# Kernel tuning notes

Hardware: AMD Instinct MI355X
Metric: run time of the kernel (lower is better)

The kernel has to match this reference:

```python
import jax, jax.numpy as jnp
import numpy as np

N_NODES = 100000
N_EDGES = 1600000
D_IN = 128
D_OUT = 128
EPS = 1e-5


def setup_inputs() -> dict:
    key = jax.random.key(0)
    ks = jax.random.split(key, 5)
    x = jax.random.normal(ks[0], (N_NODES, D_IN), dtype=jnp.float32)
    edge_index = jax.random.randint(ks[1], (2, N_EDGES), 0, N_NODES, dtype=jnp.int64)
    scale = 1.0 / np.sqrt(D_IN)
    W_root = jax.random.normal(ks[2], (D_IN, D_OUT), dtype=jnp.float32) * scale
    W_rel = jax.random.normal(ks[3], (D_IN, D_OUT), dtype=jnp.float32) * scale
    b_rel = jax.random.normal(ks[4], (D_OUT,), dtype=jnp.float32) * 0.01
    gamma = jnp.ones((D_OUT,), dtype=jnp.float32)
    beta = jnp.zeros((D_OUT,), dtype=jnp.float32)
    return {"x": x, "edge_index": edge_index, "W_root": W_root, "W_rel": W_rel,
            "b_rel": b_rel, "gamma": gamma, "beta": beta}


def reference(x, edge_index, W_root, W_rel, b_rel, gamma, beta):
    # GraphConv: out = aggr(x_j) @ W_rel + b_rel + x @ W_root   (aggr = sum)
    src = edge_index[0]
    dst = edge_index[1]
    aggr = jax.ops.segment_sum(x[src], dst, num_segments=x.shape[0])  # [N, D_IN]
    h = aggr @ W_rel + b_rel + x @ W_root                              # [N, D_OUT]
    # NodeLevelBatchNorm (training mode: batch stats over node dim, biased var)
    mean = jnp.mean(h, axis=0)
    var = jnp.mean(jnp.square(h - mean), axis=0)
    h_norm = (h - mean) * jax.lax.rsqrt(var + EPS) * gamma + beta
    return jax.nn.relu(h_norm)
```

## Files before the change

### kernel.cpp

```cpp
#include <hip/hip_runtime.h>

#define N_NODES 100000
#define N_EDGES 1600000
#define D 128
#define NB 196
#define EPT 10
#define CHUNK 2560
#define BIN_BLOCKS 625
#define CVT_X_BLOCKS 6250
#define ZROW N_NODES
#define PBK 13312

typedef __bf16 bf16x8 __attribute__((ext_vector_type(8)));
typedef float f32x4 __attribute__((ext_vector_type(4)));

__device__ __forceinline__ unsigned f2bf(float f) {
    unsigned u = __float_as_uint(f);
    return (u + 0x7fffu + ((u >> 16) & 1u)) >> 16;
}
__device__ __forceinline__ float bf_lo(unsigned u) { return __uint_as_float(u << 16); }
__device__ __forceinline__ float bf_hi(unsigned u) { return __uint_as_float(u & 0xffff0000u); }

__global__ __launch_bounds__(256) void prep_kernel(const float* __restrict__ x,
                                                   const float* __restrict__ Wrel,
                                                   const float* __restrict__ Wroot,
                                                   const int* __restrict__ ei,
                                                   unsigned short* __restrict__ x_bf,
                                                   unsigned short* __restrict__ Wt,
                                                   int* __restrict__ bcount) {
    __shared__ int h[256];
    int b = blockIdx.x;
    int t = threadIdx.x;
    if (b < CVT_X_BLOCKS) {
        size_t i = ((size_t)b * 256 + t) * 8;
        float4 v0 = *(const float4*)(x + i);
        float4 v1 = *(const float4*)(x + i + 4);
        uint4 p;
        p.x = f2bf(v0.x) | (f2bf(v0.y) << 16);
        p.y = f2bf(v0.z) | (f2bf(v0.w) << 16);
        p.z = f2bf(v1.x) | (f2bf(v1.y) << 16);
        p.w = f2bf(v1.z) | (f2bf(v1.w) << 16);
        *(uint4*)(x_bf + i) = p;
    } else if (b < CVT_X_BLOCKS + 128) {
        int c = b - CVT_X_BLOCKS;
        float v = (t < 128) ? Wrel[t * D + c] : Wroot[(t - 128) * D + c];
        Wt[c * 256 + t] = (unsigned short)f2bf(v);
    } else if (b == CVT_X_BLOCKS + 128) {
        if (t < 16) *(uint4*)(x_bf + (size_t)ZROW * D + t * 8) = make_uint4(0, 0, 0, 0);
    } else {
        int blk = b - (CVT_X_BLOCKS + 129);
        h[t] = 0;
        __syncthreads();
        int base = blk * CHUNK;
#pragma unroll
        for (int i = 0; i < EPT; ++i) {
            int dst = ei[N_EDGES + base + i * 256 + t];
            atomicAdd(&h[dst >> 9], 1);
        }
        __syncthreads();
        if (t < NB && h[t]) atomicAdd(&bcount[t], h[t]);
    }
}

__global__ __launch_bounds__(256) void bscan_kernel(const int* __restrict__ bcount,
                                                    int* __restrict__ bucket_base,
                                                    int* __restrict__ bcur) {
    __shared__ int s[256];
    int t = threadIdx.x;
    int v = (t < NB) ? bcount[t] : 0;
    s[t] = v;
    __syncthreads();
    for (int off = 1; off < 256; off <<= 1) {
        int a = (t >= off) ? s[t - off] : 0;
        __syncthreads();
        s[t] += a;
        __syncthreads();
    }
    int excl = s[t] - v;
    if (t < NB) {
        bucket_base[t] = excl;
        bcur[t] = excl;
    }
    if (t == NB) bucket_base[NB] = N_EDGES;
}

__global__ __launch_bounds__(256) void binify_kernel(const int* __restrict__ ei,
                                                     int* __restrict__ bcur,
                                                     unsigned* __restrict__ epk) {
    __shared__ int lhist[256];
    __shared__ int lstart[256];
    __shared__ int lfill[256];
    __shared__ int gbase[256];
    __shared__ uint2 stage[CHUNK];

    int t = threadIdx.x;
    int base = blockIdx.x * CHUNK;
    lhist[t] = 0;
    lfill[t] = 0;
    __syncthreads();

    int src[EPT], dst[EPT];
#pragma unroll
    for (int i = 0; i < EPT; ++i) {
        int e = base + i * 256 + t;
        src[i] = ei[e];
        dst[i] = ei[N_EDGES + e];
        atomicAdd(&lhist[dst[i] >> 9], 1);
    }
    __syncthreads();

    int v = lhist[t];
    lstart[t] = v;
    __syncthreads();
    for (int off = 1; off < 256; off <<= 1) {
        int a = (t >= off) ? lstart[t - off] : 0;
        __syncthreads();
        lstart[t] += a;
        __syncthreads();
    }
    int excl = lstart[t] - v;
    if (t < NB && v > 0) gbase[t] = atomicAdd(&bcur[t], v);
    __syncthreads();
    lstart[t] = excl;
    __syncthreads();

#pragma unroll
    for (int i = 0; i < EPT; ++i) {
        int b = dst[i] >> 9;
        int lp = atomicAdd(&lfill[b], 1);
        stage[lstart[b] + lp] = make_uint2((unsigned)src[i], (unsigned)dst[i]);
    }
    __syncthreads();

    for (int i = t; i < CHUNK; i += 256) {
        uint2 p = stage[i];
        int b = (int)(p.y >> 9);
        unsigned code = p.x | ((p.y & 511u) << 17);
        epk[gbase[b] + (i - lstart[b])] = code;
    }
}

__global__ __launch_bounds__(256) void place_kernel(const unsigned* __restrict__ epk,
                                                    const int* __restrict__ bucket_base,
                                                    int* __restrict__ rbeg,
                                                    int* __restrict__ rend,
                                                    int* __restrict__ srcs) {
    __shared__ int cnt[512];
    __shared__ int sA[512];
    __shared__ int sB[512];
    __shared__ int cursor[512];
    int b = blockIdx.x;
    int t = threadIdx.x;
    int pbeg = bucket_base[b];
    int pend = bucket_base[b + 1];
    int R = b * PBK;

    cnt[t] = 0;
    cnt[t + 256] = 0;
    __syncthreads();
    for (int i = pbeg + t; i < pend; i += 256)
        atomicAdd(&cnt[epk[i] >> 17], 1);
    __syncthreads();

    for (int j = t; j < 512; j += 256) sA[j] = j ? ((cnt[j - 1] + 7) & ~7) : 0;
    __syncthreads();
    int* cur = sA;
    int* nxt = sB;
    for (int off = 1; off < 512; off <<= 1) {
        for (int j = t; j < 512; j += 256)
            nxt[j] = cur[j] + ((j >= off) ? cur[j - off] : 0);
        __syncthreads();
        int* tm = cur; cur = nxt; nxt = tm;
    }

    for (int j = t; j < 512; j += 256) {
        int pj = (cnt[j] + 7) & ~7;
        int s = R + cur[j];
        int g = (b << 9) + j;
        if (g < 100352) { rbeg[g] = s; rend[g] = s + pj; }
        cursor[j] = s;
    }
    __syncthreads();

    for (int i = pbeg + t; i < pend; i += 256) {
        unsigned code = epk[i];
        int pos = atomicAdd(&cursor[code >> 17], 1);
        srcs[pos] = (int)(code & 0x1FFFFu);
    }
    __syncthreads();

    for (int j = t; j < 512; j += 256) {
        int endp = R + cur[j] + ((cnt[j] + 7) & ~7);
        for (int p = cursor[j]; p < endp; ++p) srcs[p] = ZROW;
    }
}

__global__ __launch_bounds__(256) void fused_gemm(const unsigned short* __restrict__ x_bf,
                                                  const int* __restrict__ rbeg,
                                                  const int* __restrict__ rend,
                                                  const int* __restrict__ srcs,
                                                  const unsigned short* __restrict__ Wt,
                                                  const float* __restrict__ brel,
                                                  unsigned short* __restrict__ h_bf,
                                                  float* __restrict__ gsum,
                                                  float* __restrict__ gss) {
    __shared__ unsigned short Af[2048 * 8];
    __shared__ unsigned short Bf[2048 * 8];
    __shared__ float sbias[128];
    __shared__ float SredS[4][128];
    __shared__ float SredQ[4][128];

    const int t = threadIdx.x;
    const int wave = t >> 6;
    const int lane = t & 63;
    const int quad = lane >> 4;
    const int l16 = lane & 15;
    const int blockRow = blockIdx.x * 128;

    if (t < 128) sbias[t] = brel[t];

#pragma unroll
    for (int f = t; f < 2048; f += 256) {
        int kcl = f >> 9;
        int ct = (f >> 6) & 7;
        int ln = f & 63;
        int col = ct * 16 + (ln & 15);
        int kb = kcl * 32 + ((ln >> 4) << 3);
        *(uint4*)&Bf[f * 8] = *(const uint4*)(Wt + col * 256 + kb);
    }

    const unsigned short* xp = x_bf + l16 * 8;
#pragma unroll 1
    for (int g = 0; g < 8; ++g) {
        int r = wave * 32 + g * 4 + quad;
        int node = blockRow + r;
        int e = rbeg[node];
        int end = rend[node];
        float a0 = 0.f, a1 = 0.f, a2 = 0.f, a3 = 0.f;
        float a4 = 0.f, a5 = 0.f, a6 = 0.f, a7 = 0.f;
        for (; e < end; e += 8) {
            int4 s0 = *(const int4*)(srcs + e);
            int4 s1 = *(const int4*)(srcs + e + 4);
            uint4 u0 = *(const uint4*)(xp + (size_t)s0.x * D);
            uint4 u1 = *(const uint4*)(xp + (size_t)s0.y * D);
            uint4 u2 = *(const uint4*)(xp + (size_t)s0.z * D);
            uint4 u3 = *(const uint4*)(xp + (size_t)s0.w * D);
            uint4 u4 = *(const uint4*)(xp + (size_t)s1.x * D);
            uint4 u5 = *(const uint4*)(xp + (size_t)s1.y * D);
            uint4 u6 = *(const uint4*)(xp + (size_t)s1.z * D);
            uint4 u7 = *(const uint4*)(xp + (size_t)s1.w * D);
            a0 += bf_lo(u0.x) + bf_lo(u1.x) + bf_lo(u2.x) + bf_lo(u3.x)
                + bf_lo(u4.x) + bf_lo(u5.x) + bf_lo(u6.x) + bf_lo(u7.x);
            a1 += bf_hi(u0.x) + bf_hi(u1.x) + bf_hi(u2.x) + bf_hi(u3.x)
                + bf_hi(u4.x) + bf_hi(u5.x) + bf_hi(u6.x) + bf_hi(u7.x);
            a2 += bf_lo(u0.y) + bf_lo(u1.y) + bf_lo(u2.y) + bf_lo(u3.y)
                + bf_lo(u4.y) + bf_lo(u5.y) + bf_lo(u6.y) + bf_lo(u7.y);
            a3 += bf_hi(u0.y) + bf_hi(u1.y) + bf_hi(u2.y) + bf_hi(u3.y)
                + bf_hi(u4.y) + bf_hi(u5.y) + bf_hi(u6.y) + bf_hi(u7.y);
            a4 += bf_lo(u0.z) + bf_lo(u1.z) + bf_lo(u2.z) + bf_lo(u3.z)
                + bf_lo(u4.z) + bf_lo(u5.z) + bf_lo(u6.z) + bf_lo(u7.z);
            a5 += bf_hi(u0.z) + bf_hi(u1.z) + bf_hi(u2.z) + bf_hi(u3.z)
                + bf_hi(u4.z) + bf_hi(u5.z) + bf_hi(u6.z) + bf_hi(u7.z);
            a6 += bf_lo(u0.w) + bf_lo(u1.w) + bf_lo(u2.w) + bf_lo(u3.w)
                + bf_lo(u4.w) + bf_lo(u5.w) + bf_lo(u6.w) + bf_lo(u7.w);
            a7 += bf_hi(u0.w) + bf_hi(u1.w) + bf_hi(u2.w) + bf_hi(u3.w)
                + bf_hi(u4.w) + bf_hi(u5.w) + bf_hi(u6.w) + bf_hi(u7.w);
        }
        uint4 w;
        w.x = f2bf(a0) | (f2bf(a1) << 16);
        w.y = f2bf(a2) | (f2bf(a3) << 16);
        w.z = f2bf(a4) | (f2bf(a5) << 16);
        w.w = f2bf(a6) | (f2bf(a7) << 16);
        int c = l16;
        int wf = ((r >> 5) << 3) + (((r >> 4) & 1) << 2) + (c >> 2);
        int L = ((c & 3) << 4) + (r & 15);
        *(uint4*)&Af[(wf * 64 + L) * 8] = w;
    }
    __syncthreads();

    f32x4 acc[2][8];
#pragma unroll
    for (int i = 0; i < 2; ++i)
#pragma unroll
        for (int j = 0; j < 8; ++j) acc[i][j] = (f32x4){0.f, 0.f, 0.f, 0.f};

#pragma unroll
    for (int kcl = 0; kcl < 4; ++kcl) {
        bf16x8 af0 = *(const bf16x8*)&Af[(((wave << 3) + kcl) * 64 + lane) * 8];
        bf16x8 af1 = *(const bf16x8*)&Af[(((wave << 3) + 4 + kcl) * 64 + lane) * 8];
#pragma unroll
        for (int ct = 0; ct < 8; ++ct) {
            bf16x8 bfrag = *(const bf16x8*)&Bf[((kcl * 8 + ct) * 64 + lane) * 8];
            acc[0][ct] = __builtin_amdgcn_mfma_f32_16x16x32_bf16(af0, bfrag, acc[0][ct], 0, 0, 0);
            acc[1][ct] = __builtin_amdgcn_mfma_f32_16x16x32_bf16(af1, bfrag, acc[1][ct], 0, 0, 0);
        }
    }
    __syncthreads();

#pragma unroll
    for (int f = t; f < 2048; f += 256) {
        int kcl = f >> 9;
        int ct = (f >> 6) & 7;
        int ln = f & 63;
        int col = ct * 16 + (ln & 15);
        int kb = 128 + kcl * 32 + ((ln >> 4) << 3);
        *(uint4*)&Bf[f * 8] = *(const uint4*)(Wt + col * 256 + kb);
    }
    __syncthreads();

    const int rowb = blockRow + wave * 32;
#pragma unroll
    for (int kcl = 0; kcl < 4; ++kcl) {
        const int k0 = kcl * 32 + quad * 8;
        bf16x8 af0 = *(const bf16x8*)(x_bf + (size_t)(rowb + l16) * D + k0);
        bf16x8 af1 = *(const bf16x8*)(x_bf + (size_t)(rowb + 16 + l16) * D + k0);
#pragma unroll
        for (int ct = 0; ct < 8; ++ct) {
            bf16x8 bfrag = *(const bf16x8*)&Bf[((kcl * 8 + ct) * 64 + lane) * 8];
            acc[0][ct] = __builtin_amdgcn_mfma_f32_16x16x32_bf16(af0, bfrag, acc[0][ct], 0, 0, 0);
            acc[1][ct] = __builtin_amdgcn_mfma_f32_16x16x32_bf16(af1, bfrag, acc[1][ct], 0, 0, 0);
        }
    }

    float csum[8], css[8];
#pragma unroll
    for (int ct = 0; ct < 8; ++ct) { csum[ct] = 0.f; css[ct] = 0.f; }

#pragma unroll
    for (int rt = 0; rt < 2; ++rt) {
#pragma unroll
        for (int ct = 0; ct < 8; ++ct) {
            int col = ct * 16 + l16;
            float bv = sbias[col];
#pragma unroll
            for (int reg = 0; reg < 4; ++reg) {
                int row = blockRow + wave * 32 + rt * 16 + quad * 4 + reg;
                if (row < N_NODES) {
                    float v = acc[rt][ct][reg] + bv;
                    h_bf[(size_t)row * D + col] = (unsigned short)f2bf(v);
                    csum[ct] += v;
                    css[ct] += v * v;
                }
            }
        }
    }
#pragma unroll
    for (int ct = 0; ct < 8; ++ct) {
        float s = csum[ct], q = css[ct];
        s += __shfl_xor(s, 16);
        s += __shfl_xor(s, 32);
        q += __shfl_xor(q, 16);
        q += __shfl_xor(q, 32);
        if (quad == 0) {
            SredS[wave][ct * 16 + l16] = s;
            SredQ[wave][ct * 16 + l16] = q;
        }
    }
    __syncthreads();
    if (t < 128) {
        float s = SredS[0][t] + SredS[1][t] + SredS[2][t] + SredS[3][t];
        float q = SredQ[0][t] + SredQ[1][t] + SredQ[2][t] + SredQ[3][t];
        unsafeAtomicAdd(&gsum[t], s);
        unsafeAtomicAdd(&gss[t], q);
    }
}

__global__ __launch_bounds__(256) void norm_kernel(const unsigned short* __restrict__ h_bf,
                                                   float* __restrict__ out,
                                                   const float* __restrict__ gsum,
                                                   const float* __restrict__ gss,
                                                   const float* __restrict__ gamma,
                                                   const float* __restrict__ beta) {
    __shared__ float sscale[128];
    __shared__ float sshift[128];
    int t = threadIdx.x;
    if (t < 128) {
        const float inv_n = 1.0f / (float)N_NODES;
        float mean = gsum[t] * inv_n;
        float var = gss[t] * inv_n - mean * mean;
        float rs = rsqrtf(var + 1e-5f);
        float sc = gamma[t] * rs;
        sscale[t] = sc;
        sshift[t] = beta[t] - mean * sc;
    }
    __syncthreads();
    size_t e = ((size_t)blockIdx.x * 256 + t) * 4;
    if (e >= (size_t)N_NODES * D) return;
    int c = (int)(e & 127);
    uint2 u = *(const uint2*)(h_bf + e);
    float4 v;
    v.x = fmaxf(bf_lo(u.x) * sscale[c + 0] + sshift[c + 0], 0.f);
    v.y = fmaxf(bf_hi(u.x) * sscale[c + 1] + sshift[c + 1], 0.f);
    v.z = fmaxf(bf_lo(u.y) * sscale[c + 2] + sshift[c + 2], 0.f);
    v.w = fmaxf(bf_hi(u.y) * sscale[c + 3] + sshift[c + 3], 0.f);
    *(float4*)(out + e) = v;
}

extern "C" void kernel_launch(void* const* d_in, const int* in_sizes, int n_in,
                              void* d_out, int out_size, void* d_ws, size_t ws_size,
                              hipStream_t stream) {
    const float* x     = (const float*)d_in[0];
    const int*   ei    = (const int*)d_in[1];
    const float* Wroot = (const float*)d_in[2];
    const float* Wrel  = (const float*)d_in[3];
    const float* brel  = (const float*)d_in[4];
    const float* gamma = (const float*)d_in[5];
    const float* beta  = (const float*)d_in[6];
    float* out = (float*)d_out;

    unsigned short* h_bf = (unsigned short*)d_ws;
    unsigned short* x_bf = h_bf + (size_t)N_NODES * D;
    unsigned short* Wt   = x_bf + (size_t)(N_NODES + 1) * D;
    float* gsum  = (float*)(Wt + 128 * 256);
    float* gss   = gsum + 128;
    int* bcount  = (int*)(gss + 128);
    int* bucket_base = bcount + 256;
    int* bcur    = bucket_base + 256;
    int* rbeg    = bcur + 256;
    int* rend    = rbeg + 100352;
    unsigned* epk = (unsigned*)(rend + 100352);
    int* srcs    = (int*)(epk + N_EDGES);

    hipMemsetAsync(gsum, 0, 512 * sizeof(int), stream);

    prep_kernel<<<CVT_X_BLOCKS + 129 + BIN_BLOCKS, 256, 0, stream>>>(
        x, Wrel, Wroot, ei, x_bf, Wt, bcount);
    bscan_kernel<<<1, 256, 0, stream>>>(bcount, bucket_base, bcur);
    binify_kernel<<<BIN_BLOCKS, 256, 0, stream>>>(ei, bcur, epk);
    place_kernel<<<NB, 256, 0, stream>>>(epk, bucket_base, rbeg, rend, srcs);
    fused_gemm<<<(N_NODES + 127) / 128, 256, 0, stream>>>(
        x_bf, rbeg, rend, srcs, Wt, brel, h_bf, gsum, gss);
    norm_kernel<<<12500, 256, 0, stream>>>(h_bf, out, gsum, gss, gamma, beta);
}
```

Baseline: 276.4 us.

## Drop shared weight staging, read B fragments from global, swizzle A tile

Removes the 32KB shared-memory buffer for the weight matrix and has each wave load its B fragments directly from global memory (likely L2/L1 hits, since every block reads the same weights). The two extra barriers around the weight reload go away. A launch-bounds hint of 4 blocks per CU is added to raise occupancy now that LDS use is smaller. An XOR swizzle on the A-tile LDS layout is meant to cut bank conflicts. The cost is more global load traffic and latency inside the MFMA loop, plus register pressure under the tighter bound.

```diff
diff --git a/kernel.cpp b/kernel.cpp
--- a/kernel.cpp
+++ b/kernel.cpp
@@ -195,17 +195,16 @@
     }
 }
 
-__global__ __launch_bounds__(256) void fused_gemm(const unsigned short* __restrict__ x_bf,
-                                                  const int* __restrict__ rbeg,
-                                                  const int* __restrict__ rend,
-                                                  const int* __restrict__ srcs,
-                                                  const unsigned short* __restrict__ Wt,
-                                                  const float* __restrict__ brel,
-                                                  unsigned short* __restrict__ h_bf,
-                                                  float* __restrict__ gsum,
-                                                  float* __restrict__ gss) {
+__global__ __launch_bounds__(256, 4) void fused_gemm(const unsigned short* __restrict__ x_bf,
+                                                     const int* __restrict__ rbeg,
+                                                     const int* __restrict__ rend,
+                                                     const int* __restrict__ srcs,
+                                                     const unsigned short* __restrict__ Wt,
+                                                     const float* __restrict__ brel,
+                                                     unsigned short* __restrict__ h_bf,
+                                                     float* __restrict__ gsum,
+                                                     float* __restrict__ gss) {
     __shared__ unsigned short Af[2048 * 8];
-    __shared__ unsigned short Bf[2048 * 8];
     __shared__ float sbias[128];
     __shared__ float SredS[4][128];
     __shared__ float SredQ[4][128];
@@ -218,16 +217,6 @@
     const int blockRow = blockIdx.x * 128;
 
     if (t < 128) sbias[t] = brel[t];
-
-#pragma unroll
-    for (int f = t; f < 2048; f += 256) {
-        int kcl = f >> 9;
-        int ct = (f >> 6) & 7;
-        int ln = f & 63;
-        int col = ct * 16 + (ln & 15);
-        int kb = kcl * 32 + ((ln >> 4) << 3);
-        *(uint4*)&Bf[f * 8] = *(const uint4*)(Wt + col * 256 + kb);
-    }
 
     const unsigned short* xp = x_bf + l16 * 8;
 #pragma unroll 1
@@ -273,7 +262,7 @@
         w.w = f2bf(a6) | (f2bf(a7) << 16);
         int c = l16;
         int wf = ((r >> 5) << 3) + (((r >> 4) & 1) << 2) + (c >> 2);
-        int L = ((c & 3) << 4) + (r & 15);
+        int L = ((c & 3) << 4) | ((r & 15) ^ (c & 3));
         *(uint4*)&Af[(wf * 64 + L) * 8] = w;
     }
     __syncthreads();
@@ -284,29 +273,19 @@
 #pragma unroll
         for (int j = 0; j < 8; ++j) acc[i][j] = (f32x4){0.f, 0.f, 0.f, 0.f};
 
+    const int Lr = (quad << 4) | (l16 ^ quad);
+
 #pragma unroll
     for (int kcl = 0; kcl < 4; ++kcl) {
-        bf16x8 af0 = *(const bf16x8*)&Af[(((wave << 3) + kcl) * 64 + lane) * 8];
-        bf16x8 af1 = *(const bf16x8*)&Af[(((wave << 3) + 4 + kcl) * 64 + lane) * 8];
+        bf16x8 af0 = *(const bf16x8*)&Af[(((wave << 3) + kcl) * 64 + Lr) * 8];
+        bf16x8 af1 = *(const bf16x8*)&Af[(((wave << 3) + 4 + kcl) * 64 + Lr) * 8];
 #pragma unroll
         for (int ct = 0; ct < 8; ++ct) {
-            bf16x8 bfrag = *(const bf16x8*)&Bf[((kcl * 8 + ct) * 64 + lane) * 8];
+            bf16x8 bfrag = *(const bf16x8*)(Wt + (ct * 16 + l16) * 256 + kcl * 32 + quad * 8);
             acc[0][ct] = __builtin_amdgcn_mfma_f32_16x16x32_bf16(af0, bfrag, acc[0][ct], 0, 0, 0);
             acc[1][ct] = __builtin_amdgcn_mfma_f32_16x16x32_bf16(af1, bfrag, acc[1][ct], 0, 0, 0);
         }
     }
-    __syncthreads();
-
-#pragma unroll
-    for (int f = t; f < 2048; f += 256) {
-        int kcl = f >> 9;
-        int ct = (f >> 6) & 7;
-        int ln = f & 63;
-        int col = ct * 16 + (ln & 15);
-        int kb = 128 + kcl * 32 + ((ln >> 4) << 3);
-        *(uint4*)&Bf[f * 8] = *(const uint4*)(Wt + col * 256 + kb);
-    }
-    __syncthreads();
 
     const int rowb = blockRow + wave * 32;
 #pragma unroll
@@ -316,7 +295,7 @@
         bf16x8 af1 = *(const bf16x8*)(x_bf + (size_t)(rowb + 16 + l16) * D + k0);
 #pragma unroll
         for (int ct = 0; ct < 8; ++ct) {
-            bf16x8 bfrag = *(const bf16x8*)&Bf[((kcl * 8 + ct) * 64 + lane) * 8];
+            bf16x8 bfrag = *(const bf16x8*)(Wt + (ct * 16 + l16) * 256 + 128 + kcl * 32 + quad * 8);
             acc[0][ct] = __builtin_amdgcn_mfma_f32_16x16x32_bf16(af0, bfrag, acc[0][ct], 0, 0, 0);
             acc[1][ct] = __builtin_amdgcn_mfma_f32_16x16x32_bf16(af1, bfrag, acc[1][ct], 0, 0, 0);
         }
```

Result: slower. 286.1 us (+3.5%).
